# Performance work log

Measured on AMD Instinct MI355X. Metric: run time of the kernel, lower is better.

Reference implementation:

```python
import jax, jax.numpy as jnp
import numpy as np

B, N, C, H, I, ID = 4, 1024, 1024, 16, 77, 768
HD = C // H
HID = 4 * C


def _ln(t, w, b):
    m = jnp.mean(t, axis=-1, keepdims=True)
    v = jnp.mean((t - m) ** 2, axis=-1, keepdims=True)
    return (t - m) * jax.lax.rsqrt(v + 1e-5) * w + b


def _gelu(t):
    return jax.nn.gelu(t, approximate=False)


def setup_inputs() -> dict:
    key = jax.random.key(0)
    ks = iter(jax.random.split(key, 16))

    def nrm(shape, s=0.02):
        return jax.random.normal(next(ks), shape, jnp.float32) * s

    return {
        'x': jax.random.normal(next(ks), (B, N, C), jnp.float32),
        'instruct_states': jax.random.normal(next(ks), (B, I, ID), jnp.float32),
        'norm1_w': jnp.ones((C,), jnp.float32), 'norm1_b': jnp.zeros((C,), jnp.float32),
        'qkv_w': nrm((3 * C, C)),
        'q_bias': jnp.zeros((C,), jnp.float32), 'v_bias': jnp.zeros((C,), jnp.float32),
        'proj_w': nrm((C, C)), 'proj_b': jnp.zeros((C,), jnp.float32),
        'gamma_1': jnp.full((C,), 1e-5, jnp.float32), 'gamma_2': jnp.full((C,), 1e-5, jnp.float32),
        'norm2_w': jnp.ones((C,), jnp.float32), 'norm2_b': jnp.zeros((C,), jnp.float32),
        'fc1_w': nrm((HID, C)), 'fc1_b': jnp.zeros((HID,), jnp.float32),
        'fc2_w': nrm((C, HID)), 'fc2_b': jnp.zeros((C,), jnp.float32),
        'pfc1_w': nrm((HID, C)), 'pfc1_b': jnp.zeros((HID,), jnp.float32),
        'pfc2_w': nrm((C, HID)), 'pfc2_b': jnp.zeros((C,), jnp.float32),
        'parallel_gate': jnp.full((1,), 0.1, jnp.float32),
        'ir_ln_w': jnp.ones((ID,), jnp.float32), 'ir_ln_b': jnp.zeros((ID,), jnp.float32),
        'ir_l1_w': nrm((C, ID)), 'ir_l1_b': jnp.zeros((C,), jnp.float32),
        'ir_l2_w': nrm((C, C)), 'ir_l2_b': jnp.zeros((C,), jnp.float32),
    }


def reference(x, instruct_states, norm1_w, norm1_b, qkv_w, q_bias, v_bias,
              proj_w, proj_b, gamma_1, gamma_2, norm2_w, norm2_b,
              fc1_w, fc1_b, fc2_w, fc2_b, pfc1_w, pfc1_b, pfc2_w, pfc2_b,
              parallel_gate, ir_ln_w, ir_ln_b, ir_l1_w, ir_l1_b, ir_l2_w, ir_l2_b):
    # instruct_dim_reduce: LN -> Linear -> GELU -> Linear
    kv = _ln(instruct_states, ir_ln_w, ir_ln_b)
    kv = _gelu(kv @ ir_l1_w.T + ir_l1_b) @ ir_l2_w.T + ir_l2_b  # [B, I, C]

    xn = _ln(x, norm1_w, norm1_b)                               # [B, N, C]
    cat = jnp.concatenate([kv, xn], axis=1)                     # [B, I+N, C]
    S = I + N

    qkv_bias = jnp.concatenate([q_bias, jnp.zeros_like(v_bias), v_bias])
    qkv = (cat @ qkv_w.T + qkv_bias).reshape(B, S, 3, H, HD)
    q = qkv[:, :, 0].transpose(0, 2, 1, 3)                      # [B, H, S, HD]
    k = qkv[:, :, 1].transpose(0, 2, 1, 3)
    v = qkv[:, :, 2].transpose(0, 2, 1, 3)

    # only visual queries, keys/values over instructions + visual tokens
    q = q[:, :, I:, :] * (HD ** -0.5)                           # [B, H, N, HD]
    attn = jnp.einsum('bhqd,bhkd->bhqk', q, k)                  # [B, H, N, S]
    attn = jax.nn.softmax(attn, axis=-1)
    o = jnp.einsum('bhqk,bhkd->bqhd', attn, v).reshape(B, N, C)
    o = o @ proj_w.T + proj_b

    x = x + gamma_1 * o                                         # LayerScale residual

    y = _ln(x, norm2_w, norm2_b)
    mlp = _gelu(y @ fc1_w.T + fc1_b) @ fc2_w.T + fc2_b
    pmlp = _gelu(y @ pfc1_w.T + pfc1_b) @ pfc2_w.T + pfc2_b
    x = x + gamma_2 * mlp + parallel_gate * pmlp
    return x
```

## Files before the change

### kernel.cpp

```cpp
#include <hip/hip_runtime.h>
#include <cstdint>

#define Bv   4
#define Nv   1024
#define Cv   1024
#define Hv   16
#define Iv   77
#define IDv  768
#define HDv  64
#define HIDv 4096
#define Sv   (Iv + Nv)
#define BIv  (Bv * Iv)
#define BSv  (Bv * Sv)
#define BNv  (Bv * Nv)
#define SPADv 1152

typedef __bf16 bf16x8_t __attribute__((ext_vector_type(8)));
typedef float  f32x4_t  __attribute__((ext_vector_type(4)));
typedef unsigned short us8_t __attribute__((ext_vector_type(8)));
typedef long  l2_t  __attribute__((ext_vector_type(2)));
typedef int   i32x4_t __attribute__((ext_vector_type(4)));
typedef int   i32x8_t __attribute__((ext_vector_type(8)));

__device__ inline f32x4_t zero4() { f32x4_t z; z[0]=0.f; z[1]=0.f; z[2]=0.f; z[3]=0.f; return z; }

__device__ inline unsigned short f2bf(float f) {
    unsigned int u = __builtin_bit_cast(unsigned int, f);
    u = (u + 0x7fffu + ((u >> 16) & 1u)) >> 16;
    return (unsigned short)u;
}
__device__ inline float bf2f(unsigned short u) {
    return __builtin_bit_cast(float, ((unsigned int)u) << 16);
}
__device__ inline unsigned int f4_fp8(float a, float b, float c, float d) {
    int v = __builtin_amdgcn_cvt_pk_fp8_f32(a, b, 0, false);
    v = __builtin_amdgcn_cvt_pk_fp8_f32(c, d, v, true);
    return (unsigned int)v;
}

__device__ inline float gelu_f(float x) {
    float u = 0.7978845608f * x * (1.0f + 0.044715f * x * x);
    float e = __expf(2.0f * u);
    float t = 1.0f - 2.0f / (e + 1.0f);
    return 0.5f * x * (1.0f + t);
}

__device__ inline void gload_lds16(const void* g, void* l) {
    __builtin_amdgcn_global_load_lds(
        (__attribute__((address_space(1))) void*)(unsigned long long)g,
        (__attribute__((address_space(3))) void*)(unsigned long long)l,
        16, 0, 0);
}

__device__ inline i32x8_t frag32(const unsigned char* p0, const unsigned char* p1) {
    i32x4_t lo = *(const i32x4_t*)p0;
    i32x4_t hi = *(const i32x4_t*)p1;
    i32x8_t r;
    r[0] = lo[0]; r[1] = lo[1]; r[2] = lo[2]; r[3] = lo[3];
    r[4] = hi[0]; r[5] = hi[1]; r[6] = hi[2]; r[7] = hi[3];
    return r;
}

__global__ __launch_bounds__(256) void cvt8_kernel(
        const float* s0, const float* s1, const float* s2, const float* s3,
        const float* s4, const float* s5, const float* s6, const float* s7,
        void* d0, void* d1, void* d2, void* d3,
        void* d4, void* d5, void* d6, void* d7,
        const float* g1, const float* g2, const float* gate) {
    (void)g1;
    long i = (long)blockIdx.x * 256 + threadIdx.x;
    const float* src; void* dst; long off;
    const float* sptr = nullptr; int K4 = 1; float wmul = 1.0f; bool f8 = false;
    if (i < 2097152) {
        if (i < 786432)       { src = s0; dst = d0; off = i; f8 = true; wmul = 32.f; }
        else if (i < 1048576) { src = s1; dst = d1; off = i - 786432;  f8 = true; wmul = 32.f; }
        else                  { src = s2; dst = d2; off = i - 1048576; f8 = true; wmul = 32.f; }
    } else if (i < 4194304) {
        if (i < 3145728)      { src = s3; dst = d3; off = i - 2097152; f8 = true; wmul = 32.f; sptr = g2; K4 = 1024; }
        else                  { src = s4; dst = d4; off = i - 3145728; f8 = true; wmul = 32.f; }
    } else {
        if (i < 5242880)      { src = s5; dst = d5; off = i - 4194304; f8 = true; wmul = 32.f; sptr = gate; K4 = 0x7fffffff; }
        else if (i < 5439488) { src = s6; dst = d6; off = i - 5242880; }
        else                  { src = s7; dst = d7; off = i - 5439488; }
    }
    float sc = (sptr ? sptr[(int)(off / K4)] : 1.0f) * wmul;
    float4 v = ((const float4*)src)[off];
    if (f8) {
        ((unsigned int*)dst)[off] = f4_fp8(v.x * sc, v.y * sc, v.z * sc, v.w * sc);
    } else {
        ushort4 o = {f2bf(v.x * sc), f2bf(v.y * sc), f2bf(v.z * sc), f2bf(v.w * sc)};
        ((ushort4*)dst)[off] = o;
    }
}

__global__ __launch_bounds__(256) void bias_prep_kernel(
        const float* __restrict__ qb, const float* __restrict__ vb,
        const float* __restrict__ fc2b, const float* __restrict__ pfc2b,
        const float* __restrict__ projb_in,
        const float* __restrict__ fc1b, const float* __restrict__ pfc1b,
        const float* __restrict__ g1, const float* __restrict__ g2,
        const float* __restrict__ gate,
        float* __restrict__ qkvb, float* __restrict__ bfuse,
        float* __restrict__ projb, float* __restrict__ bcat) {
    int i = blockIdx.x * 256 + threadIdx.x;
    if (i < 3 * Cv) {
        float v = 0.f;
        if (i < Cv) v = qb[i];
        else if (i >= 2 * Cv) v = vb[i - 2 * Cv];
        qkvb[i] = v;
    } else if (i < 4 * Cv) {
        int n = i - 3 * Cv;
        bfuse[n] = g2[n] * fc2b[n] + gate[0] * pfc2b[n];
    } else if (i < 5 * Cv) {
        int n = i - 4 * Cv;
        projb[n] = g1[n] * projb_in[n];
    } else if (i < 13 * Cv) {
        int j = i - 5 * Cv;
        bcat[j] = (j < HIDv) ? fc1b[j] : pfc1b[j - HIDv];
    }
}

template <int F8>
__global__ __launch_bounds__(256) void ln_kernel(const float* __restrict__ in,
                                                 const float* __restrict__ w,
                                                 const float* __restrict__ bvec,
                                                 void* __restrict__ out,
                                                 int cols, float invcols,
                                                 int div_, int stride_, int off_) {
    const int r = blockIdx.x;
    const int tid = threadIdx.x;
    const float* row = in + (size_t)r * cols;
    float s = 0.f, s2 = 0.f;
    for (int c = tid * 4; c < cols; c += 1024) {
        float4 v = *(const float4*)(row + c);
        s  += v.x + v.y + v.z + v.w;
        s2 += v.x * v.x + v.y * v.y + v.z * v.z + v.w * v.w;
    }
#pragma unroll
    for (int o2 = 32; o2 > 0; o2 >>= 1) { s += __shfl_down(s, o2); s2 += __shfl_down(s2, o2); }
    __shared__ float sh[10];
    const int lane = tid & 63, wave = tid >> 6;
    if (lane == 0) { sh[wave] = s; sh[4 + wave] = s2; }
    __syncthreads();
    if (tid == 0) {
        float S1 = sh[0] + sh[1] + sh[2] + sh[3];
        float S2 = sh[4] + sh[5] + sh[6] + sh[7];
        float mean = S1 * invcols;
        float var  = S2 * invcols - mean * mean;
        sh[8] = mean;
        sh[9] = rsqrtf(var + 1e-5f);
    }
    __syncthreads();
    const float mean = sh[8], rstd = sh[9];
    const size_t orow = (size_t)((r / div_) * stride_ + (r % div_) + off_) * cols;
    for (int c = tid * 4; c < cols; c += 1024) {
        float4 v  = *(const float4*)(row + c);
        float4 wv = *(const float4*)(w + c);
        float4 bv = *(const float4*)(bvec + c);
        float o0 = (v.x - mean) * rstd * wv.x + bv.x;
        float o1 = (v.y - mean) * rstd * wv.y + bv.y;
        float o2 = (v.z - mean) * rstd * wv.z + bv.z;
        float o3 = (v.w - mean) * rstd * wv.w + bv.w;
        if constexpr (F8) {
            *(unsigned int*)((unsigned char*)out + orow + c) =
                f4_fp8(o0 * 16.f, o1 * 16.f, o2 * 16.f, o3 * 16.f);
        } else {
            ushort4 o = {f2bf(o0), f2bf(o1), f2bf(o2), f2bf(o3)};
            *(ushort4*)((unsigned short*)out + orow + c) = o;
        }
    }
}

__global__ __launch_bounds__(256) void proj_ln2_kernel(
        const unsigned short* __restrict__ parts,
        const float* __restrict__ x,
        const float* __restrict__ projb,
        const float* __restrict__ g1,
        const float* __restrict__ w, const float* __restrict__ bvec,
        float* __restrict__ x1, unsigned char* __restrict__ y8) {
    const int r = blockIdx.x;
    const int tid = threadIdx.x;
    const int c = tid * 4;
    const size_t base = (size_t)r * Cv + c;
    float4 xv = *(const float4*)(x + base);
    float4 pb = *(const float4*)(projb + c);
    float4 gv = *(const float4*)(g1 + c);
    ushort4 u0 = *(const ushort4*)(parts + base);
    ushort4 u1 = *(const ushort4*)(parts + (size_t)BNv * Cv + base);
    float4 v;
    v.x = xv.x + pb.x + gv.x * (bf2f(u0.x) + bf2f(u1.x));
    v.y = xv.y + pb.y + gv.y * (bf2f(u0.y) + bf2f(u1.y));
    v.z = xv.z + pb.z + gv.z * (bf2f(u0.z) + bf2f(u1.z));
    v.w = xv.w + pb.w + gv.w * (bf2f(u0.w) + bf2f(u1.w));
    *(float4*)(x1 + base) = v;

    float s  = v.x + v.y + v.z + v.w;
    float s2 = v.x * v.x + v.y * v.y + v.z * v.z + v.w * v.w;
#pragma unroll
    for (int o2 = 32; o2 > 0; o2 >>= 1) { s += __shfl_down(s, o2); s2 += __shfl_down(s2, o2); }
    __shared__ float sh[10];
    const int lane = tid & 63, wave = tid >> 6;
    if (lane == 0) { sh[wave] = s; sh[4 + wave] = s2; }
    __syncthreads();
    if (tid == 0) {
        float S1 = sh[0] + sh[1] + sh[2] + sh[3];
        float S2 = sh[4] + sh[5] + sh[6] + sh[7];
        float mean = S1 * (1.0f / Cv);
        float var  = S2 * (1.0f / Cv) - mean * mean;
        sh[8] = mean;
        sh[9] = rsqrtf(var + 1e-5f);
    }
    __syncthreads();
    const float mean = sh[8], rstd = sh[9];
    float4 wv = *(const float4*)(w + c);
    float4 bv = *(const float4*)(bvec + c);
    float o0 = (v.x - mean) * rstd * wv.x + bv.x;
    float o1 = (v.y - mean) * rstd * wv.y + bv.y;
    float o2 = (v.z - mean) * rstd * wv.z + bv.z;
    float o3 = (v.w - mean) * rstd * wv.w + bv.w;
    *(unsigned int*)(y8 + base) = f4_fp8(o0 * 16.f, o1 * 16.f, o2 * 16.f, o3 * 16.f);
}

template <int MODE>
__global__ __launch_bounds__(256) void gemm_tiny_kernel(
        const unsigned short* __restrict__ A,
        const unsigned short* __restrict__ W,
        const float* __restrict__ bias,
        unsigned short* __restrict__ outp,
        int M, int N, int K) {
    const int lane = threadIdx.x & 63;
    const int wave = threadIdx.x >> 6;
    const int m16  = lane & 15;
    const int g4   = lane >> 4;
    const int wid  = blockIdx.x * 4 + wave;
    const int ntiles = N >> 6;
    const int mti = wid / ntiles;
    if (mti * 16 >= M + 15) return;
    const int m0 = mti * 16;
    const int n0 = (wid % ntiles) * 64;

    int am = m0 + m16; if (am > M - 1) am = M - 1;
    const unsigned short* ap = A + (size_t)am * K + g4 * 8;
    const unsigned short* wp = W + (size_t)(n0 + m16) * K + g4 * 8;

    f32x4_t acc[4];
#pragma unroll
    for (int a = 0; a < 4; ++a) acc[a] = zero4();

#pragma unroll 2
    for (int kk = 0; kk < K; kk += 32) {
        bf16x8_t xf = *(const bf16x8_t*)(ap + kk);
#pragma unroll
        for (int a = 0; a < 4; ++a) {
            bf16x8_t wf = *(const bf16x8_t*)(wp + (size_t)a * 16 * K + kk);
            acc[a] = __builtin_amdgcn_mfma_f32_16x16x32_bf16(wf, xf, acc[a], 0, 0, 0);
        }
    }

    const int r = m0 + m16;
    if (r >= M) return;
#pragma unroll
    for (int a = 0; a < 4; ++a) {
        const int cb = n0 + a * 16 + g4 * 4;
        const float4 bv4 = *(const float4*)(bias + cb);
        const float v0 = acc[a][0] + bv4.x;
        const float v1 = acc[a][1] + bv4.y;
        const float v2 = acc[a][2] + bv4.z;
        const float v3 = acc[a][3] + bv4.w;
        if constexpr (MODE == 1) {
            ushort4 o = {f2bf(gelu_f(v0)), f2bf(gelu_f(v1)),
                         f2bf(gelu_f(v2)), f2bf(gelu_f(v3))};
            *(ushort4*)(outp + (size_t)r * N + cb) = o;
        } else {
            const int rr2 = (r / Iv) * Sv + (r % Iv);
            *(unsigned int*)((unsigned char*)outp + (size_t)rr2 * Cv + cb) =
                f4_fp8(v0 * 16.f, v1 * 16.f, v2 * 16.f, v3 * 16.f);
        }
    }
}

__global__ __launch_bounds__(256) void gemm_fp8_bf16out_kernel(
        const unsigned char* __restrict__ A,
        const unsigned char* __restrict__ W,
        const float* __restrict__ bias,
        unsigned short* __restrict__ outp,
        int M, int N, int K) {
    __shared__ unsigned char As[2][128 * 128];
    __shared__ unsigned char Bs[2][128 * 128];
    const int tid  = threadIdx.x;
    const int lane = tid & 63;
    const int wave = tid >> 6;
    const int m16  = lane & 15;
    const int g4   = lane >> 4;
    const int n0 = blockIdx.x * 128;
    const int m0 = blockIdx.y * 128;
    const int wm = (wave >> 1) * 64;
    const int wn = (wave & 1) * 64;

    const int rowin = tid >> 3;
    const int sslot = (tid & 7) ^ (rowin & 7);
    const unsigned char* agp[4];
#pragma unroll
    for (int j = 0; j < 4; ++j) {
        int gr = m0 + j * 32 + rowin; if (gr > M - 1) gr = M - 1;
        agp[j] = A + (size_t)gr * K + sslot * 16;
    }
    const unsigned char* bgp = W + (size_t)(n0 + rowin) * K + sslot * 16;

    const int sw = m16 & 7;
    const int ra0 = ((2 * g4) ^ sw) * 16;
    const int ra1 = ((2 * g4 + 1) ^ sw) * 16;

    f32x4_t acc[4][4];
#pragma unroll
    for (int a = 0; a < 4; ++a)
#pragma unroll
        for (int bb = 0; bb < 4; ++bb) acc[a][bb] = zero4();

    auto stage = [&](int buf) {
#pragma unroll
        for (int j = 0; j < 4; ++j) {
            gload_lds16(agp[j], &As[buf][j * 4096 + wave * 1024]);
            gload_lds16(bgp + (size_t)j * 32 * K, &Bs[buf][j * 4096 + wave * 1024]);
            agp[j] += 128;
        }
        bgp += 128;
    };

    stage(0);
    const int NIT = K >> 7;
    for (int it = 0; it < NIT; ++it) {
        const int cur = it & 1;
        __syncthreads();
        if (it + 1 < NIT) stage(cur ^ 1);
        i32x8_t xv[4], wv[4];
#pragma unroll
        for (int bb = 0; bb < 4; ++bb) {
            const unsigned char* rb = &As[cur][(wm + bb * 16 + m16) * 128];
            xv[bb] = frag32(rb + ra0, rb + ra1);
        }
#pragma unroll
        for (int a = 0; a < 4; ++a) {
            const unsigned char* rb = &Bs[cur][(wn + a * 16 + m16) * 128];
            wv[a] = frag32(rb + ra0, rb + ra1);
        }
#pragma unroll
        for (int a = 0; a < 4; ++a)
#pragma unroll
            for (int bb = 0; bb < 4; ++bb)
                acc[a][bb] = __builtin_amdgcn_mfma_scale_f32_16x16x128_f8f6f4(
                    wv[a], xv[bb], acc[a][bb], 0, 0, 0, 0x7f7f7f7f, 0, 0x7f7f7f7f);
    }

    const float ds = 1.0f / 512.0f;
#pragma unroll
    for (int a = 0; a < 4; ++a) {
        const int cb = n0 + wn + a * 16 + g4 * 4;
        const float4 bv4 = *(const float4*)(bias + cb);
#pragma unroll
        for (int bb = 0; bb < 4; ++bb) {
            const int r = m0 + wm + bb * 16 + m16;
            if (r < M) {
                const size_t idx = (size_t)r * N + cb;
                ushort4 o = {f2bf(acc[a][bb][0] * ds + bv4.x),
                             f2bf(acc[a][bb][1] * ds + bv4.y),
                             f2bf(acc[a][bb][2] * ds + bv4.z),
                             f2bf(acc[a][bb][3] * ds + bv4.w)};
                *(ushort4*)(outp + idx) = o;
            }
        }
    }
}

__global__ __launch_bounds__(256) void gemm_fp8_gelu_kernel(
        const unsigned char* __restrict__ A,
        const unsigned char* __restrict__ W,
        const float* __restrict__ bias,
        unsigned char* __restrict__ outp,
        int M, int N, int K) {
    __shared__ unsigned char As[2][128 * 128];
    __shared__ unsigned char Bs[2][128 * 128];
    const int tid  = threadIdx.x;
    const int lane = tid & 63;
    const int wave = tid >> 6;
    const int m16  = lane & 15;
    const int g4   = lane >> 4;
    const int bid = blockIdx.x;
    const int xcd = bid & 7, l = bid >> 3;
    const int by = (xcd << 2) | (l & 3);
    const int bx = l >> 2;
    const int n0 = bx * 128;
    const int m0 = by * 128;
    const int wm = (wave >> 1) * 64;
    const int wn = (wave & 1) * 64;

    const int rowin = tid >> 3;
    const int sslot = (tid & 7) ^ (rowin & 7);
    const unsigned char* agp = A + (size_t)(m0 + rowin) * K + sslot * 16;
    const unsigned char* bgp = W + (size_t)(n0 + rowin) * K + sslot * 16;

    const int sw = m16 & 7;
    const int ra0 = ((2 * g4) ^ sw) * 16;
    const int ra1 = ((2 * g4 + 1) ^ sw) * 16;

    f32x4_t acc[4][4];
#pragma unroll
    for (int a = 0; a < 4; ++a)
#pragma unroll
        for (int bb = 0; bb < 4; ++bb) acc[a][bb] = zero4();

    auto stage = [&](int buf) {
#pragma unroll
        for (int j = 0; j < 4; ++j) {
            gload_lds16(agp + (size_t)j * 32 * K, &As[buf][j * 4096 + wave * 1024]);
            gload_lds16(bgp + (size_t)j * 32 * K, &Bs[buf][j * 4096 + wave * 1024]);
        }
        agp += 128; bgp += 128;
    };

    stage(0);
    const int NIT = K >> 7;
    for (int it = 0; it < NIT; ++it) {
        const int cur = it & 1;
        __syncthreads();
        if (it + 1 < NIT) stage(cur ^ 1);
        i32x8_t xv[4], wv[4];
#pragma unroll
        for (int bb = 0; bb < 4; ++bb) {
            const unsigned char* rb = &As[cur][(wm + bb * 16 + m16) * 128];
            xv[bb] = frag32(rb + ra0, rb + ra1);
        }
#pragma unroll
        for (int a = 0; a < 4; ++a) {
            const unsigned char* rb = &Bs[cur][(wn + a * 16 + m16) * 128];
            wv[a] = frag32(rb + ra0, rb + ra1);
        }
#pragma unroll
        for (int a = 0; a < 4; ++a)
#pragma unroll
            for (int bb = 0; bb < 4; ++bb)
                acc[a][bb] = __builtin_amdgcn_mfma_scale_f32_16x16x128_f8f6f4(
                    wv[a], xv[bb], acc[a][bb], 0, 0, 0, 0x7f7f7f7f, 0, 0x7f7f7f7f);
    }

    const float ds = 1.0f / 512.0f;
#pragma unroll
    for (int a = 0; a < 4; ++a) {
        const int cb = n0 + wn + a * 16 + g4 * 4;
        const float4 bv4 = *(const float4*)(bias + cb);
#pragma unroll
        for (int bb = 0; bb < 4; ++bb) {
            const int r = m0 + wm + bb * 16 + m16;
            const size_t idx = (size_t)r * N + cb;
            unsigned int pk = f4_fp8(gelu_f(acc[a][bb][0] * ds + bv4.x) * 16.f,
                                     gelu_f(acc[a][bb][1] * ds + bv4.y) * 16.f,
                                     gelu_f(acc[a][bb][2] * ds + bv4.z) * 16.f,
                                     gelu_f(acc[a][bb][3] * ds + bv4.w) * 16.f);
            *(unsigned int*)(outp + idx) = pk;
        }
    }
}

__global__ __launch_bounds__(256) void gemm_fp8_splitk_kernel(
        const unsigned char* __restrict__ A1,
        const unsigned char* __restrict__ W1,
        const unsigned char* __restrict__ A2,
        const unsigned char* __restrict__ W2,
        unsigned short* __restrict__ parts,
        int M, int N, int lda, int ldw, int Kc, int zsplit) {
    __shared__ unsigned char As[2][128 * 128];
    __shared__ unsigned char Bs[2][128 * 128];
    const int tid  = threadIdx.x;
    const int lane = tid & 63;
    const int wave = tid >> 6;
    const int m16  = lane & 15;
    const int g4   = lane >> 4;
    const int bid = blockIdx.x;
    const int xcd = bid & 7, l = bid >> 3;
    const int by = (xcd << 2) | (l & 3);
    const int rr = l >> 2;
    const int bx = rr & 7;
    const int z  = rr >> 3;
    const int n0 = bx * 128;
    const int m0 = by * 128;
    const int wm = (wave >> 1) * 64;
    const int wn = (wave & 1) * 64;

    const unsigned char* A = (z < zsplit) ? A1 : A2;
    const unsigned char* W = (z < zsplit) ? W1 : W2;
    const int k0 = (z % zsplit) * Kc;

    const int rowin = tid >> 3;
    const int sslot = (tid & 7) ^ (rowin & 7);
    const unsigned char* agp = A + (size_t)(m0 + rowin) * lda + k0 + sslot * 16;
    const unsigned char* bgp = W + (size_t)(n0 + rowin) * ldw + k0 + sslot * 16;

    const int sw = m16 & 7;
    const int ra0 = ((2 * g4) ^ sw) * 16;
    const int ra1 = ((2 * g4 + 1) ^ sw) * 16;

    f32x4_t acc[4][4];
#pragma unroll
    for (int a = 0; a < 4; ++a)
#pragma unroll
        for (int bb = 0; bb < 4; ++bb) acc[a][bb] = zero4();

    auto stage = [&](int buf) {
#pragma unroll
        for (int j = 0; j < 4; ++j) {
            gload_lds16(agp + (size_t)j * 32 * lda, &As[buf][j * 4096 + wave * 1024]);
            gload_lds16(bgp + (size_t)j * 32 * ldw, &Bs[buf][j * 4096 + wave * 1024]);
        }
        agp += 128; bgp += 128;
    };

    stage(0);
    const int NIT = Kc >> 7;
    for (int it = 0; it < NIT; ++it) {
        const int cur = it & 1;
        __syncthreads();
        if (it + 1 < NIT) stage(cur ^ 1);
        i32x8_t xv[4], wv[4];
#pragma unroll
        for (int bb = 0; bb < 4; ++bb) {
            const unsigned char* rb = &As[cur][(wm + bb * 16 + m16) * 128];
            xv[bb] = frag32(rb + ra0, rb + ra1);
        }
#pragma unroll
        for (int a = 0; a < 4; ++a) {
            const unsigned char* rb = &Bs[cur][(wn + a * 16 + m16) * 128];
            wv[a] = frag32(rb + ra0, rb + ra1);
        }
#pragma unroll
        for (int a = 0; a < 4; ++a)
#pragma unroll
            for (int bb = 0; bb < 4; ++bb)
                acc[a][bb] = __builtin_amdgcn_mfma_scale_f32_16x16x128_f8f6f4(
                    wv[a], xv[bb], acc[a][bb], 0, 0, 0, 0x7f7f7f7f, 0, 0x7f7f7f7f);
    }

    unsigned short* pz = parts + (size_t)z * M * N;
    const float ds = 1.0f / 512.0f;
#pragma unroll
    for (int a = 0; a < 4; ++a) {
        const int cb = n0 + wn + a * 16 + g4 * 4;
#pragma unroll
        for (int bb = 0; bb < 4; ++bb) {
            const int r = m0 + wm + bb * 16 + m16;
            const size_t idx = (size_t)r * N + cb;
            ushort4 o = {f2bf(acc[a][bb][0] * ds), f2bf(acc[a][bb][1] * ds),
                         f2bf(acc[a][bb][2] * ds), f2bf(acc[a][bb][3] * ds)};
            *(ushort4*)(pz + idx) = o;
        }
    }
}

template <int NP>
__global__ __launch_bounds__(256) void reduce_kernel(
        const unsigned short* __restrict__ parts,
        const float* __restrict__ resid,
        const float* __restrict__ bias,
        float* __restrict__ out, int MN, int N4mask) {
    int i = blockIdx.x * 256 + threadIdx.x;
    if (i * 4 >= MN) return;
    float4 res = ((const float4*)resid)[i];
    float4 bv  = *(const float4*)(bias + (i & N4mask) * 4);
    float4 o = {res.x + bv.x, res.y + bv.y, res.z + bv.z, res.w + bv.w};
#pragma unroll
    for (int z = 0; z < NP; ++z) {
        ushort4 u = ((const ushort4*)(parts + (size_t)z * MN))[i];
        o.x += bf2f(u.x); o.y += bf2f(u.y); o.z += bf2f(u.z); o.w += bf2f(u.w);
    }
    ((float4*)out)[i] = o;
}

__global__ __launch_bounds__(256) void vtrans_kernel(const unsigned short* __restrict__ qkv,
                                                     unsigned short* __restrict__ vt) {
    __shared__ unsigned short Vs[64 * 64];
    const int stile = blockIdx.x;
    const int bh = blockIdx.y;
    const int b = bh >> 4, h = bh & 15;
    const int tid = threadIdx.x;
#pragma unroll
    for (int j = 0; j < 2; ++j) {
        int c = j * 256 + tid;
        int r = c >> 3, d8 = (c & 7) * 8;
        int s = stile * 64 + r;
        uint4 v = {0u, 0u, 0u, 0u};
        if (s < Sv) v = *(const uint4*)(qkv + ((size_t)(b * Sv + s) * 3 + 2) * Cv + h * 64 + d8);
        *(uint4*)&Vs[r * 64 + d8] = v;
    }
    __syncthreads();
    const int d  = tid >> 2;
    const int p0 = (tid & 3) * 16;
    unsigned short tmp[16];
#pragma unroll
    for (int e = 0; e < 16; ++e) {
        int p = p0 + e;
        int s_local = (p & 32) + 16 * ((p >> 2) & 1) + 4 * ((p & 31) >> 3) + (p & 3);
        tmp[e] = Vs[s_local * 64 + d];
    }
    unsigned short* dst = vt + ((size_t)bh * 64 + d) * SPADv + stile * 64 + p0;
    *(uint4*)dst       = *(const uint4*)&tmp[0];
    *(uint4*)(dst + 8) = *(const uint4*)&tmp[8];
}

__global__ __launch_bounds__(256) void attn_kernel(const unsigned short* __restrict__ qkv,
                                                   const unsigned short* __restrict__ vt,
                                                   unsigned char* __restrict__ o) {
    __shared__ unsigned short Qs[64 * 64];
    __shared__ unsigned short Ks[2][64 * 64];
    __shared__ unsigned short Vts[2][64 * 64];

    const int tid  = threadIdx.x;
    const int lane = tid & 63;
    const int wave = tid >> 6;
    const int m16  = lane & 15;
    const int g4   = lane >> 4;
    const int qt = blockIdx.x;
    const int bh = blockIdx.y;
    const int b = bh >> 4, h = bh & 15;

    const int lr = lane >> 3;
    const int csw = ((lane & 7) ^ lr) * 8;
    const int sw7 = m16 & 7;

#pragma unroll
    for (int j = 0; j < 2; ++j) {
        int r = wave * 16 + j * 8 + lr;
        int s = Iv + qt * 64 + r;
        gload_lds16(qkv + ((size_t)(b * Sv + s) * 3) * Cv + h * 64 + csw,
                    &Qs[(wave * 16 + j * 8) * 64]);
    }

    auto stage_kv = [&](int st, int buf) {
#pragma unroll
        for (int j = 0; j < 2; ++j) {
            int r = wave * 16 + j * 8 + lr;
            int s = st * 64 + r; if (s > Sv - 1) s = Sv - 1;
            gload_lds16(qkv + ((size_t)(b * Sv + s) * 3 + 1) * Cv + h * 64 + csw,
                        &Ks[buf][(wave * 16 + j * 8) * 64]);
            gload_lds16(vt + ((size_t)bh * 64 + r) * SPADv + st * 64 + csw,
                        &Vts[buf][(wave * 16 + j * 8) * 64]);
        }
    };

    f32x4_t oacc[4];
#pragma unroll
    for (int dt = 0; dt < 4; ++dt) oacc[dt] = zero4();
    float m_run = -1e30f, l_run = 0.f;

    stage_kv(0, 0);
    __syncthreads();

    const bf16x8_t qf0 = *(const bf16x8_t*)&Qs[(wave * 16 + m16) * 64 + ((g4 ^ sw7) * 8)];
    const bf16x8_t qf1 = *(const bf16x8_t*)&Qs[(wave * 16 + m16) * 64 + (((4 + g4) ^ sw7) * 8)];

    const int NT = (Sv + 63) / 64;
    for (int st = 0; st < NT; ++st) {
        const int cur = st & 1;
        if (st + 1 < NT) stage_kv(st + 1, cur ^ 1);

        f32x4_t sc[4];
        __builtin_amdgcn_s_setprio(1);
#pragma unroll
        for (int kt = 0; kt < 4; ++kt) {
            bf16x8_t k0 = *(const bf16x8_t*)&Ks[cur][(kt * 16 + m16) * 64 + ((g4 ^ sw7) * 8)];
            bf16x8_t k1 = *(const bf16x8_t*)&Ks[cur][(kt * 16 + m16) * 64 + (((4 + g4) ^ sw7) * 8)];
            f32x4_t z = zero4();
            z = __builtin_amdgcn_mfma_f32_16x16x32_bf16(k0, qf0, z, 0, 0, 0);
            z = __builtin_amdgcn_mfma_f32_16x16x32_bf16(k1, qf1, z, 0, 0, 0);
            sc[kt] = z;
        }
        __builtin_amdgcn_s_setprio(0);

        float mx = -1e30f;
#pragma unroll
        for (int kt = 0; kt < 4; ++kt)
#pragma unroll
            for (int r = 0; r < 4; ++r) {
                int key = st * 64 + kt * 16 + g4 * 4 + r;
                float v = sc[kt][r] * 0.125f;
                v = (key < Sv) ? v : -1e30f;
                sc[kt][r] = v;
                mx = fmaxf(mx, v);
            }
        mx = fmaxf(mx, __shfl_xor(mx, 16));
        mx = fmaxf(mx, __shfl_xor(mx, 32));
        const float mnew  = fmaxf(m_run, mx);
        const float alpha = __expf(m_run - mnew);
        m_run = mnew;
        float sum = 0.f;
#pragma unroll
        for (int kt = 0; kt < 4; ++kt)
#pragma unroll
            for (int r = 0; r < 4; ++r) {
                float p = __expf(sc[kt][r] - mnew);
                sc[kt][r] = p;
                sum += p;
            }
        sum += __shfl_xor(sum, 16);
        sum += __shfl_xor(sum, 32);
        l_run = l_run * alpha + sum;
#pragma unroll
        for (int dt = 0; dt < 4; ++dt) oacc[dt] *= alpha;

        us8_t pu0, pu1;
#pragma unroll
        for (int j = 0; j < 8; ++j) {
            pu0[j] = f2bf(sc[(j >> 2)][j & 3]);
            pu1[j] = f2bf(sc[2 + (j >> 2)][j & 3]);
        }
        const bf16x8_t pf0 = __builtin_bit_cast(bf16x8_t, pu0);
        const bf16x8_t pf1 = __builtin_bit_cast(bf16x8_t, pu1);

        __builtin_amdgcn_s_setprio(1);
#pragma unroll
        for (int dt = 0; dt < 4; ++dt) {
            bf16x8_t v0 = *(const bf16x8_t*)&Vts[cur][(dt * 16 + m16) * 64 + ((g4 ^ sw7) * 8)];
            bf16x8_t v1 = *(const bf16x8_t*)&Vts[cur][(dt * 16 + m16) * 64 + (((4 + g4) ^ sw7) * 8)];
            oacc[dt] = __builtin_amdgcn_mfma_f32_16x16x32_bf16(v0, pf0, oacc[dt], 0, 0, 0);
            oacc[dt] = __builtin_amdgcn_mfma_f32_16x16x32_bf16(v1, pf1, oacc[dt], 0, 0, 0);
        }
        __builtin_amdgcn_s_setprio(0);
        __syncthreads();
    }

    const float inv16 = 16.0f / l_run;
    const int q = qt * 64 + wave * 16 + m16;
    const size_t row = (size_t)(b * Nv + q) * Cv + h * 64;
#pragma unroll
    for (int dt = 0; dt < 4; ++dt) {
        *(unsigned int*)&o[row + dt * 16 + g4 * 4] =
            f4_fp8(oacc[dt][0] * inv16, oacc[dt][1] * inv16,
                   oacc[dt][2] * inv16, oacc[dt][3] * inv16);
    }
}

extern "C" void kernel_launch(void* const* d_in, const int* in_sizes, int n_in,
                              void* d_out, int out_size, void* d_ws, size_t ws_size,
                              hipStream_t stream) {
    (void)in_sizes; (void)n_in; (void)out_size; (void)ws_size;
    const float* x       = (const float*)d_in[0];
    const float* instr   = (const float*)d_in[1];
    const float* norm1_w = (const float*)d_in[2];
    const float* norm1_b = (const float*)d_in[3];
    const float* qkv_w   = (const float*)d_in[4];
    const float* q_bias  = (const float*)d_in[5];
    const float* v_bias  = (const float*)d_in[6];
    const float* proj_w  = (const float*)d_in[7];
    const float* proj_b  = (const float*)d_in[8];
    const float* gamma_1 = (const float*)d_in[9];
    const float* gamma_2 = (const float*)d_in[10];
    const float* norm2_w = (const float*)d_in[11];
    const float* norm2_b = (const float*)d_in[12];
    const float* fc1_w   = (const float*)d_in[13];
    const float* fc1_b   = (const float*)d_in[14];
    const float* fc2_w   = (const float*)d_in[15];
    const float* fc2_b   = (const float*)d_in[16];
    const float* pfc1_w  = (const float*)d_in[17];
    const float* pfc1_b  = (const float*)d_in[18];
    const float* pfc2_w  = (const float*)d_in[19];
    const float* pfc2_b  = (const float*)d_in[20];
    const float* gate    = (const float*)d_in[21];
    const float* ir_ln_w = (const float*)d_in[22];
    const float* ir_ln_b = (const float*)d_in[23];
    const float* ir_l1_w = (const float*)d_in[24];
    const float* ir_l1_b = (const float*)d_in[25];
    const float* ir_l2_w = (const float*)d_in[26];
    const float* ir_l2_b = (const float*)d_in[27];
    float* out = (float*)d_out;

    char* ws = (char*)d_ws;
    size_t off = 0;
    auto alloc = [&](size_t bytes) -> char* {
        char* p = ws + off;
        off += (bytes + 255) & ~(size_t)255;
        return p;
    };
    unsigned char*  w_qkv8 = (unsigned char*)alloc((size_t)3 * Cv * Cv);
    unsigned char*  w_proj8= (unsigned char*)alloc((size_t)Cv * Cv);
    unsigned char*  w_mlp1 = (unsigned char*)alloc((size_t)2 * HIDv * Cv);
    unsigned char*  w_fc2  = (unsigned char*)alloc((size_t)Cv * HIDv);
    unsigned char*  w_pfc2 = (unsigned char*)alloc((size_t)Cv * HIDv);
    unsigned short* w_ir1  = (unsigned short*)alloc((size_t)Cv * IDv * 2);
    unsigned short* w_ir2  = (unsigned short*)alloc((size_t)Cv * Cv * 2);
    float*          qkvb   = (float*)alloc((size_t)3 * Cv * 4);
    float*          bfuse  = (float*)alloc((size_t)Cv * 4);
    float*          projb  = (float*)alloc((size_t)Cv * 4);
    float*          bcat   = (float*)alloc((size_t)2 * HIDv * 4);
    unsigned short* irln   = (unsigned short*)alloc((size_t)BIv * IDv * 2);
    unsigned short* h1     = (unsigned short*)alloc((size_t)BIv * Cv * 2);
    unsigned char*  cat8   = (unsigned char*)alloc((size_t)BSv * Cv);
    unsigned short* qkvbuf = (unsigned short*)alloc((size_t)BSv * 3 * Cv * 2);
    unsigned char*  obuf8  = (unsigned char*)alloc((size_t)BNv * Cv);
    float*          x1     = (float*)alloc((size_t)BNv * Cv * 4);
    unsigned char*  ybuf8  = (unsigned char*)alloc((size_t)BNv * Cv);
    unsigned char*  gbufA  = (unsigned char*)alloc((size_t)BNv * 2 * HIDv);
    unsigned short* fpart  = (unsigned short*)alloc((size_t)2 * BNv * Cv * 2);
    unsigned short* vt     = (unsigned short*)gbufA;
    unsigned short* ppart  = fpart;

    cvt8_kernel<<<22272, 256, 0, stream>>>(qkv_w, proj_w, fc1_w, fc2_w, pfc1_w, pfc2_w,
                                           ir_l1_w, ir_l2_w,
                                           w_qkv8, w_proj8, w_mlp1, w_fc2,
                                           w_mlp1 + (size_t)HIDv * Cv, w_pfc2,
                                           w_ir1, w_ir2,
                                           gamma_1, gamma_2, gate);

    bias_prep_kernel<<<52, 256, 0, stream>>>(q_bias, v_bias, fc2_b, pfc2_b, proj_b,
                                             fc1_b, pfc1_b,
                                             gamma_1, gamma_2, gate,
                                             qkvb, bfuse, projb, bcat);

    ln_kernel<0><<<BIv, 256, 0, stream>>>(instr, ir_ln_w, ir_ln_b, irln,
                                          IDv, 1.0f / IDv, 1 << 28, 0, 0);
    ln_kernel<1><<<BNv, 256, 0, stream>>>(x, norm1_w, norm1_b, cat8,
                                          Cv, 1.0f / Cv, Nv, Sv, Iv);
    {
        const int wtiles = ((BIv + 15) / 16) * (Cv / 64);
        gemm_tiny_kernel<1><<<(wtiles + 3) / 4, 256, 0, stream>>>(
            irln, w_ir1, ir_l1_b, h1, BIv, Cv, IDv);
        gemm_tiny_kernel<2><<<(wtiles + 3) / 4, 256, 0, stream>>>(
            h1, w_ir2, ir_l2_b, (unsigned short*)cat8, BIv, Cv, Cv);
    }

    gemm_fp8_bf16out_kernel<<<dim3(3 * Cv / 128, (BSv + 127) / 128), 256, 0, stream>>>(
        cat8, w_qkv8, qkvb, qkvbuf, BSv, 3 * Cv, Cv);

    vtrans_kernel<<<dim3(18, Bv * Hv), 256, 0, stream>>>(qkvbuf, vt);
    attn_kernel<<<dim3(Nv / 64, Bv * Hv), 256, 0, stream>>>(qkvbuf, vt, obuf8);

    gemm_fp8_splitk_kernel<<<512, 256, 0, stream>>>(
        obuf8, w_proj8, obuf8, w_proj8, ppart,
        BNv, Cv, Cv, Cv, Cv / 2, 2);
    proj_ln2_kernel<<<BNv, 256, 0, stream>>>(
        ppart, x, projb, gamma_1, norm2_w, norm2_b, x1, ybuf8);

    gemm_fp8_gelu_kernel<<<2048, 256, 0, stream>>>(
        ybuf8, w_mlp1, bcat, gbufA, BNv, 2 * HIDv, Cv);

    gemm_fp8_splitk_kernel<<<512, 256, 0, stream>>>(
        gbufA, w_fc2, gbufA + HIDv, w_pfc2, fpart,
        BNv, Cv, 2 * HIDv, HIDv, HIDv, 1);
    reduce_kernel<2><<<(BNv * Cv / 4 + 255) / 256, 256, 0, stream>>>(
        fpart, x1, bfuse, out, BNv * Cv, Cv / 4 - 1);
}
```

Measured before the change: 453.6 us.

## Persist MLP1 GEMM blocks over four N-tiles and process 128 queries per attention block

The fused fc1/pfc1 GELU GEMM now launches 512 blocks, and each block loops over four output column tiles with K fixed at 1024. It writes each tile's epilogue and zeroes the accumulators before moving on, which reuses the A rows across tiles and cuts block launch overhead. The attention kernel now handles 128 queries per block (two 16-row groups per wave), loading Q fragments straight from global memory into registers. Each K/V tile staged in LDS is therefore used for twice as many queries, halving K/V traffic, at the cost of more registers and lower occupancy. The hardcoded loop count of 32 ties the GEMM to this specific shape.

```diff
diff --git a/kernel.cpp b/kernel.cpp
--- a/kernel.cpp
+++ b/kernel.cpp
@@ -18,7 +18,6 @@
 typedef __bf16 bf16x8_t __attribute__((ext_vector_type(8)));
 typedef float  f32x4_t  __attribute__((ext_vector_type(4)));
 typedef unsigned short us8_t __attribute__((ext_vector_type(8)));
-typedef long  l2_t  __attribute__((ext_vector_type(2)));
 typedef int   i32x4_t __attribute__((ext_vector_type(4)));
 typedef int   i32x8_t __attribute__((ext_vector_type(8)));
 
@@ -387,43 +386,45 @@
     const int g4   = lane >> 4;
     const int bid = blockIdx.x;
     const int xcd = bid & 7, l = bid >> 3;
-    const int by = (xcd << 2) | (l & 3);
-    const int bx = l >> 2;
-    const int n0 = bx * 128;
+    const int by  = (xcd << 2) | (l & 3);
+    const int bxb = l >> 2;
     const int m0 = by * 128;
     const int wm = (wave >> 1) * 64;
     const int wn = (wave & 1) * 64;
 
     const int rowin = tid >> 3;
     const int sslot = (tid & 7) ^ (rowin & 7);
-    const unsigned char* agp = A + (size_t)(m0 + rowin) * K + sslot * 16;
-    const unsigned char* bgp = W + (size_t)(n0 + rowin) * K + sslot * 16;
-
     const int sw = m16 & 7;
     const int ra0 = ((2 * g4) ^ sw) * 16;
     const int ra1 = ((2 * g4 + 1) ^ sw) * 16;
 
+    const unsigned char* arow = A + (size_t)(m0 + rowin) * K + sslot * 16;
+    const unsigned char* wrow = W + (size_t)rowin * K + sslot * 16;
+
+    auto stage_for = [&](int git, int buf) {
+        const int kk  = (git & 7) * 128;
+        const int n0t = ((git >> 3) * 16 + bxb) * 128;
+        const unsigned char* ag = arow + kk;
+        const unsigned char* bg = wrow + (size_t)n0t * K + kk;
+#pragma unroll
+        for (int j = 0; j < 4; ++j) {
+            gload_lds16(ag + (size_t)j * 32 * K, &As[buf][j * 4096 + wave * 1024]);
+            gload_lds16(bg + (size_t)j * 32 * K, &Bs[buf][j * 4096 + wave * 1024]);
+        }
+    };
+
     f32x4_t acc[4][4];
 #pragma unroll
     for (int a = 0; a < 4; ++a)
 #pragma unroll
         for (int bb = 0; bb < 4; ++bb) acc[a][bb] = zero4();
 
-    auto stage = [&](int buf) {
-#pragma unroll
-        for (int j = 0; j < 4; ++j) {
-            gload_lds16(agp + (size_t)j * 32 * K, &As[buf][j * 4096 + wave * 1024]);
-            gload_lds16(bgp + (size_t)j * 32 * K, &Bs[buf][j * 4096 + wave * 1024]);
-        }
-        agp += 128; bgp += 128;
-    };
-
-    stage(0);
-    const int NIT = K >> 7;
-    for (int it = 0; it < NIT; ++it) {
-        const int cur = it & 1;
+    const float ds = 1.0f / 512.0f;
+    stage_for(0, 0);
+    for (int git = 0; git < 32; ++git) {
+        const int cur = git & 1;
         __syncthreads();
-        if (it + 1 < NIT) stage(cur ^ 1);
+        if (git + 1 < 32) stage_for(git + 1, cur ^ 1);
         i32x8_t xv[4], wv[4];
 #pragma unroll
         for (int bb = 0; bb < 4; ++bb) {
@@ -441,22 +442,25 @@
             for (int bb = 0; bb < 4; ++bb)
                 acc[a][bb] = __builtin_amdgcn_mfma_scale_f32_16x16x128_f8f6f4(
                     wv[a], xv[bb], acc[a][bb], 0, 0, 0, 0x7f7f7f7f, 0, 0x7f7f7f7f);
-    }
-
-    const float ds = 1.0f / 512.0f;
-#pragma unroll
-    for (int a = 0; a < 4; ++a) {
-        const int cb = n0 + wn + a * 16 + g4 * 4;
-        const float4 bv4 = *(const float4*)(bias + cb);
-#pragma unroll
-        for (int bb = 0; bb < 4; ++bb) {
-            const int r = m0 + wm + bb * 16 + m16;
-            const size_t idx = (size_t)r * N + cb;
-            unsigned int pk = f4_fp8(gelu_f(acc[a][bb][0] * ds + bv4.x) * 16.f,
-                                     gelu_f(acc[a][bb][1] * ds + bv4.y) * 16.f,
-                                     gelu_f(acc[a][bb][2] * ds + bv4.z) * 16.f,
-                                     gelu_f(acc[a][bb][3] * ds + bv4.w) * 16.f);
-            *(unsigned int*)(outp + idx) = pk;
+        if ((git & 7) == 7) {
+            const int n0t = ((git >> 3) * 16 + bxb) * 128;
+#pragma unroll
+            for (int a = 0; a < 4; ++a) {
+                const int cb = n0t + wn + a * 16 + g4 * 4;
+                const float4 bv4 = *(const float4*)(bias + cb);
+#pragma unroll
+                for (int bb = 0; bb < 4; ++bb) {
+                    const int r = m0 + wm + bb * 16 + m16;
+                    const size_t idx = (size_t)r * N + cb;
+                    unsigned int pk = f4_fp8(gelu_f(acc[a][bb][0] * ds + bv4.x) * 16.f,
+                                             gelu_f(acc[a][bb][1] * ds + bv4.y) * 16.f,
+                                             gelu_f(acc[a][bb][2] * ds + bv4.z) * 16.f,
+                                             gelu_f(acc[a][bb][3] * ds + bv4.w) * 16.f);
+                    *(unsigned int*)(outp + idx) = pk;
+#pragma unroll
+                    for (int q = 0; q < 4; ++q) acc[a][bb][q] = 0.f;
+                }
+            }
         }
     }
 }
@@ -608,7 +612,6 @@
 __global__ __launch_bounds__(256) void attn_kernel(const unsigned short* __restrict__ qkv,
                                                    const unsigned short* __restrict__ vt,
                                                    unsigned char* __restrict__ o) {
-    __shared__ unsigned short Qs[64 * 64];
     __shared__ unsigned short Ks[2][64 * 64];
     __shared__ unsigned short Vts[2][64 * 64];
 
@@ -625,12 +628,13 @@
     const int csw = ((lane & 7) ^ lr) * 8;
     const int sw7 = m16 & 7;
 
-#pragma unroll
-    for (int j = 0; j < 2; ++j) {
-        int r = wave * 16 + j * 8 + lr;
-        int s = Iv + qt * 64 + r;
-        gload_lds16(qkv + ((size_t)(b * Sv + s) * 3) * Cv + h * 64 + csw,
-                    &Qs[(wave * 16 + j * 8) * 64]);
+    bf16x8_t qf0[2], qf1[2];
+#pragma unroll
+    for (int g = 0; g < 2; ++g) {
+        const int s = Iv + qt * 128 + wave * 32 + g * 16 + m16;
+        const unsigned short* qp = qkv + ((size_t)(b * Sv + s) * 3) * Cv + h * 64 + g4 * 8;
+        qf0[g] = *(const bf16x8_t*)qp;
+        qf1[g] = *(const bf16x8_t*)(qp + 32);
     }
 
     auto stage_kv = [&](int st, int buf) {
@@ -645,95 +649,113 @@
         }
     };
 
-    f32x4_t oacc[4];
-#pragma unroll
-    for (int dt = 0; dt < 4; ++dt) oacc[dt] = zero4();
-    float m_run = -1e30f, l_run = 0.f;
+    f32x4_t oaccA[4], oaccB[4];
+#pragma unroll
+    for (int dt = 0; dt < 4; ++dt) { oaccA[dt] = zero4(); oaccB[dt] = zero4(); }
+    float m_runA = -1e30f, l_runA = 0.f;
+    float m_runB = -1e30f, l_runB = 0.f;
 
     stage_kv(0, 0);
     __syncthreads();
-
-    const bf16x8_t qf0 = *(const bf16x8_t*)&Qs[(wave * 16 + m16) * 64 + ((g4 ^ sw7) * 8)];
-    const bf16x8_t qf1 = *(const bf16x8_t*)&Qs[(wave * 16 + m16) * 64 + (((4 + g4) ^ sw7) * 8)];
 
     const int NT = (Sv + 63) / 64;
     for (int st = 0; st < NT; ++st) {
         const int cur = st & 1;
         if (st + 1 < NT) stage_kv(st + 1, cur ^ 1);
 
-        f32x4_t sc[4];
-        __builtin_amdgcn_s_setprio(1);
+        bf16x8_t k0[4], k1[4];
 #pragma unroll
         for (int kt = 0; kt < 4; ++kt) {
-            bf16x8_t k0 = *(const bf16x8_t*)&Ks[cur][(kt * 16 + m16) * 64 + ((g4 ^ sw7) * 8)];
-            bf16x8_t k1 = *(const bf16x8_t*)&Ks[cur][(kt * 16 + m16) * 64 + (((4 + g4) ^ sw7) * 8)];
-            f32x4_t z = zero4();
-            z = __builtin_amdgcn_mfma_f32_16x16x32_bf16(k0, qf0, z, 0, 0, 0);
-            z = __builtin_amdgcn_mfma_f32_16x16x32_bf16(k1, qf1, z, 0, 0, 0);
-            sc[kt] = z;
-        }
-        __builtin_amdgcn_s_setprio(0);
-
-        float mx = -1e30f;
-#pragma unroll
-        for (int kt = 0; kt < 4; ++kt)
-#pragma unroll
-            for (int r = 0; r < 4; ++r) {
-                int key = st * 64 + kt * 16 + g4 * 4 + r;
-                float v = sc[kt][r] * 0.125f;
-                v = (key < Sv) ? v : -1e30f;
-                sc[kt][r] = v;
-                mx = fmaxf(mx, v);
+            k0[kt] = *(const bf16x8_t*)&Ks[cur][(kt * 16 + m16) * 64 + ((g4 ^ sw7) * 8)];
+            k1[kt] = *(const bf16x8_t*)&Ks[cur][(kt * 16 + m16) * 64 + (((4 + g4) ^ sw7) * 8)];
+        }
+        bf16x8_t v0[4], v1[4];
+#pragma unroll
+        for (int dt = 0; dt < 4; ++dt) {
+            v0[dt] = *(const bf16x8_t*)&Vts[cur][(dt * 16 + m16) * 64 + ((g4 ^ sw7) * 8)];
+            v1[dt] = *(const bf16x8_t*)&Vts[cur][(dt * 16 + m16) * 64 + (((4 + g4) ^ sw7) * 8)];
+        }
+
+#pragma unroll
+        for (int g = 0; g < 2; ++g) {
+            const bf16x8_t qa = g ? qf0[1] : qf0[0];
+            const bf16x8_t qb = g ? qf1[1] : qf1[0];
+            f32x4_t* oacc = g ? oaccB : oaccA;
+            float m_run = g ? m_runB : m_runA;
+            float l_run = g ? l_runB : l_runA;
+
+            f32x4_t sc[4];
+#pragma unroll
+            for (int kt = 0; kt < 4; ++kt) {
+                f32x4_t z = zero4();
+                z = __builtin_amdgcn_mfma_f32_16x16x32_bf16(k0[kt], qa, z, 0, 0, 0);
+                z = __builtin_amdgcn_mfma_f32_16x16x32_bf16(k1[kt], qb, z, 0, 0, 0);
+                sc[kt] = z;
             }
-        mx = fmaxf(mx, __shfl_xor(mx, 16));
-        mx = fmaxf(mx, __shfl_xor(mx, 32));
-        const float mnew  = fmaxf(m_run, mx);
-        const float alpha = __expf(m_run - mnew);
-        m_run = mnew;
-        float sum = 0.f;
-#pragma unroll
-        for (int kt = 0; kt < 4; ++kt)
-#pragma unroll
-            for (int r = 0; r < 4; ++r) {
-                float p = __expf(sc[kt][r] - mnew);
-                sc[kt][r] = p;
-                sum += p;
+
+            float mx = -1e30f;
+#pragma unroll
+            for (int kt = 0; kt < 4; ++kt)
+#pragma unroll
+                for (int r = 0; r < 4; ++r) {
+                    int key = st * 64 + kt * 16 + g4 * 4 + r;
+                    float v = sc[kt][r] * 0.125f;
+                    v = (key < Sv) ? v : -1e30f;
+                    sc[kt][r] = v;
+                    mx = fmaxf(mx, v);
+                }
+            mx = fmaxf(mx, __shfl_xor(mx, 16));
+            mx = fmaxf(mx, __shfl_xor(mx, 32));
+            const float mnew  = fmaxf(m_run, mx);
+            const float alpha = __expf(m_run - mnew);
+            m_run = mnew;
+            float sum = 0.f;
+#pragma unroll
+            for (int kt = 0; kt < 4; ++kt)
+#pragma unroll
+                for (int r = 0; r < 4; ++r) {
+                    float p = __expf(sc[kt][r] - mnew);
+                    sc[kt][r] = p;
+                    sum += p;
+                }
+            sum += __shfl_xor(sum, 16);
+            sum += __shfl_xor(sum, 32);
+            l_run = l_run * alpha + sum;
+#pragma unroll
+            for (int dt = 0; dt < 4; ++dt) oacc[dt] *= alpha;
+
+            us8_t pu0, pu1;
+#pragma unroll
+            for (int j = 0; j < 8; ++j) {
+                pu0[j] = f2bf(sc[(j >> 2)][j & 3]);
+                pu1[j] = f2bf(sc[2 + (j >> 2)][j & 3]);
             }
-        sum += __shfl_xor(sum, 16);
-        sum += __shfl_xor(sum, 32);
-        l_run = l_run * alpha + sum;
-#pragma unroll
-        for (int dt = 0; dt < 4; ++dt) oacc[dt] *= alpha;
-
-        us8_t pu0, pu1;
-#pragma unroll
-        for (int j = 0; j < 8; ++j) {
-            pu0[j] = f2bf(sc[(j >> 2)][j & 3]);
-            pu1[j] = f2bf(sc[2 + (j >> 2)][j & 3]);
-        }
-        const bf16x8_t pf0 = __builtin_bit_cast(bf16x8_t, pu0);
-        const bf16x8_t pf1 = __builtin_bit_cast(bf16x8_t, pu1);
-
-        __builtin_amdgcn_s_setprio(1);
+            const bf16x8_t pf0 = __builtin_bit_cast(bf16x8_t, pu0);
+            const bf16x8_t pf1 = __builtin_bit_cast(bf16x8_t, pu1);
+
+#pragma unroll
+            for (int dt = 0; dt < 4; ++dt) {
+                oacc[dt] = __builtin_amdgcn_mfma_f32_16x16x32_bf16(v0[dt], pf0, oacc[dt], 0, 0, 0);
+                oacc[dt] = __builtin_amdgcn_mfma_f32_16x16x32_bf16(v1[dt], pf1, oacc[dt], 0, 0, 0);
+            }
+            if (g) { m_runB = m_run; l_runB = l_run; }
+            else   { m_runA = m_run; l_runA = l_run; }
+        }
+        __syncthreads();
+    }
+
+#pragma unroll
+    for (int g = 0; g < 2; ++g) {
+        const f32x4_t* oacc = g ? oaccB : oaccA;
+        const float inv16 = 16.0f / (g ? l_runB : l_runA);
+        const int q = qt * 128 + wave * 32 + g * 16 + m16;
+        const size_t row = (size_t)(b * Nv + q) * Cv + h * 64;
 #pragma unroll
         for (int dt = 0; dt < 4; ++dt) {
-            bf16x8_t v0 = *(const bf16x8_t*)&Vts[cur][(dt * 16 + m16) * 64 + ((g4 ^ sw7) * 8)];
-            bf16x8_t v1 = *(const bf16x8_t*)&Vts[cur][(dt * 16 + m16) * 64 + (((4 + g4) ^ sw7) * 8)];
-            oacc[dt] = __builtin_amdgcn_mfma_f32_16x16x32_bf16(v0, pf0, oacc[dt], 0, 0, 0);
-            oacc[dt] = __builtin_amdgcn_mfma_f32_16x16x32_bf16(v1, pf1, oacc[dt], 0, 0, 0);
-        }
-        __builtin_amdgcn_s_setprio(0);
-        __syncthreads();
-    }
-
-    const float inv16 = 16.0f / l_run;
-    const int q = qt * 64 + wave * 16 + m16;
-    const size_t row = (size_t)(b * Nv + q) * Cv + h * 64;
-#pragma unroll
-    for (int dt = 0; dt < 4; ++dt) {
-        *(unsigned int*)&o[row + dt * 16 + g4 * 4] =
-            f4_fp8(oacc[dt][0] * inv16, oacc[dt][1] * inv16,
-                   oacc[dt][2] * inv16, oacc[dt][3] * inv16);
+            *(unsigned int*)&o[row + dt * 16 + g4 * 4] =
+                f4_fp8(oacc[dt][0] * inv16, oacc[dt][1] * inv16,
+                       oacc[dt][2] * inv16, oacc[dt][3] * inv16);
+        }
     }
 }
 
@@ -829,7 +851,7 @@
         cat8, w_qkv8, qkvb, qkvbuf, BSv, 3 * Cv, Cv);
 
     vtrans_kernel<<<dim3(18, Bv * Hv), 256, 0, stream>>>(qkvbuf, vt);
-    attn_kernel<<<dim3(Nv / 64, Bv * Hv), 256, 0, stream>>>(qkvbuf, vt, obuf8);
+    attn_kernel<<<dim3(Nv / 128, Bv * Hv), 256, 0, stream>>>(qkvbuf, vt, obuf8);
 
     gemm_fp8_splitk_kernel<<<512, 256, 0, stream>>>(
         obuf8, w_proj8, obuf8, w_proj8, ppart,
@@ -837,7 +859,7 @@
     proj_ln2_kernel<<<BNv, 256, 0, stream>>>(
         ppart, x, projb, gamma_1, norm2_w, norm2_b, x1, ybuf8);
 
-    gemm_fp8_gelu_kernel<<<2048, 256, 0, stream>>>(
+    gemm_fp8_gelu_kernel<<<512, 256, 0, stream>>>(
         ybuf8, w_mlp1, bcat, gbufA, BNv, 2 * HIDv, Cv);
 
     gemm_fp8_splitk_kernel<<<512, 256, 0, stream>>>(
```

Measured after the change: 454.4 us. Within noise of the previous version (+0.2%).
